# Performance work log

Hardware: AMD Instinct MI355X
Metric: run time of the kernel (lower is better)

The kernel has to match this reference:

```python
import jax, jax.numpy as jnp
import numpy as np

D = 256
H = 4
L = 6
N = 32768
VOCAB = 256
EPS = 1e-5  # torch LayerNorm default


def ln(x):
    # LayerNorm over last dim, no affine (elementwise_affine=False)
    m = x.mean(-1, keepdims=True)
    v = ((x - m) ** 2).mean(-1, keepdims=True)
    return (x - m) * jax.lax.rsqrt(v + EPS)


def rope(x):
    # standard rotary embedding over last dim (interleaved pairs), base 10000
    d = x.shape[-1]
    T = x.shape[-2]
    inv_freq = 1.0 / (10000.0 ** (jnp.arange(0, d, 2, dtype=jnp.float32) / d))
    ang = jnp.arange(T, dtype=jnp.float32)[:, None] * inv_freq[None, :]  # [T, d/2]
    cos, sin = jnp.cos(ang), jnp.sin(ang)
    x1, x2 = x[..., 0::2], x[..., 1::2]
    r1 = x1 * cos - x2 * sin
    r2 = x1 * sin + x2 * cos
    return jnp.stack([r1, r2], axis=-1).reshape(x.shape)


def setup_inputs() -> dict:
    key = jax.random.key(0)
    ks = jax.random.split(key, 6)
    B, T = 2, 1024
    idx = jax.random.randint(ks[0], (B, T), 0, VOCAB)
    std = 0.02
    wte = jax.random.normal(ks[1], (VOCAB, D), jnp.float32) * std
    encoder = jax.random.normal(ks[2], (N, D), jnp.float32) * std
    decoder_x = jax.random.normal(ks[3], (H, D, N // H), jnp.float32) * std
    decoder_y = jax.random.normal(ks[4], (H, D, N // H), jnp.float32) * std
    readout = jax.random.normal(ks[5], (D, VOCAB), jnp.float32) * std
    return {"idx": idx, "wte": wte, "encoder": encoder,
            "decoder_x": decoder_x, "decoder_y": decoder_y, "readout": readout}


def reference(idx, wte, encoder, decoder_x, decoder_y, readout):
    B, T = idx.shape
    v_ast = ln(wte[idx])[:, None]  # [B,1,T,D]
    # strictly-lower-triangular causal mask: tril(diagonal=-1)
    mask = jnp.tril(jnp.ones((T, T), dtype=bool), -1)
    for _ in range(L):
        # x: [B,H,T,N/H]
        x = jax.nn.relu(jnp.einsum('bltd,hdn->bhtn', v_ast, decoder_x))
        qr = rope(x)
        kr = rope(x)
        # raw dot-product scores, no softmax; strictly causal mask
        scores = jnp.einsum('bhtn,bhsn->bhts', qr, kr)  # [B,H,T,T]
        scores = jnp.where(mask, scores, 0.0)
        a_ast = jnp.einsum('bhts,blsd->bhtd', scores, v_ast)  # [B,H,T,D]
        y = jax.nn.relu(jnp.einsum('bhtd,hdn->bhtn', ln(a_ast), decoder_y)) * x
        y = jnp.transpose(y, (0, 2, 1, 3)).reshape(B, 1, T, N)  # [B,1,T,N]
        # dropout is identity in eval mode
        v_ast = ln(v_ast + ln(y @ encoder))
    return v_ast[:, 0] @ readout  # [B,T,VOCAB]
```

## Files before the change

### kernel.cpp

```cpp
#include <hip/hip_runtime.h>
#include <hip/hip_fp16.h>
#include <math.h>

#define D_     256
#define H_     4
#define NH     8192
#define NTOT   32768
#define T_     1024
#define B_     2
#define ROWS   2048
#define VOCAB_ 256
#define LAYERS 6
#define EPS_   1e-5f

typedef _Float16 f16;
typedef __attribute__((ext_vector_type(8))) _Float16 f16x8;
typedef __attribute__((ext_vector_type(4))) float f32x4;

#define BM 128
#define BN 128
#define BK 64
#define LDST (BK + 8)

#define EPI_F32       0
#define EPI_RELU      1
#define EPI_RELU_MUL  3
#define EPI_F32_ATOM  4
#define EPI_RELU_ROPE 5

__device__ __forceinline__ uint4 rope8(uint4 xin, uint4 csin) {
    union U { uint4 v; f16 h[8]; };
    U x, cs, o;
    x.v = xin; cs.v = csin;
#pragma unroll
    for (int j = 0; j < 4; j++) {
        float x1 = (float)x.h[2 * j], x2 = (float)x.h[2 * j + 1];
        float c  = (float)cs.h[2 * j], s = (float)cs.h[2 * j + 1];
        o.h[2 * j]     = (f16)(x1 * c - x2 * s);
        o.h[2 * j + 1] = (f16)(x1 * s + x2 * c);
    }
    return o.v;
}

template<int EPI, bool ROPE, bool ACVT>
__device__ __forceinline__ void gemm_core(
    const void* __restrict__ Av, int lda,
    const f16* __restrict__ Bt, int ldb,
    void* __restrict__ Cv, int ldc,
    int row0, int col0, int k0beg, int k_end,
    const f16* __restrict__ aux,
    const f16* __restrict__ cstab)
{
    __shared__ f16 As[BM * LDST];
    __shared__ f16 Bs[BN * LDST];

    const int tid  = threadIdx.x;
    const int lane = tid & 63;
    const int wid  = tid >> 6;
    const int wr   = (wid >> 1) * 64;
    const int wc   = (wid & 1) * 64;
    const int lr   = lane & 15;
    const int lk   = (lane >> 4) * 8;

    f32x4 acc[4][4];
#pragma unroll
    for (int m = 0; m < 4; m++)
#pragma unroll
        for (int n = 0; n < 4; n++) acc[m][n] = (f32x4){0.f, 0.f, 0.f, 0.f};

    for (int k0 = k0beg; k0 < k_end; k0 += BK) {
#pragma unroll
        for (int i = 0; i < 4; i++) {
            int v  = tid + i * 256;
            int r  = v >> 3;
            int c8 = (v & 7) << 3;
            uint4 av;
            if constexpr (ACVT) {
                const float* Af = (const float*)Av;
                size_t base = (size_t)(row0 + r) * lda + k0 + c8;
                float4 f0 = *(const float4*)(Af + base);
                float4 f1 = *(const float4*)(Af + base + 4);
                int colb = k0 + c8, row = row0 + r;
                float fv[8] = {f0.x, f0.y, f0.z, f0.w, f1.x, f1.y, f1.z, f1.w};
                union { uint4 v4; f16 h[8]; } u;
#pragma unroll
                for (int j = 0; j < 8; j++)
                    u.h[j] = (f16)((colb + j < row) ? fv[j] : 0.f);
                av = u.v4;
            } else {
                av = *(const uint4*)((const f16*)Av + (size_t)(row0 + r) * lda + k0 + c8);
                if constexpr (ROPE) {
                    int p = (k0 + c8) >> 1;
                    av = rope8(av, *(const uint4*)(cstab + ((size_t)(row0 + r) * 4096 + p) * 2));
                }
            }
            uint4 bv = *(const uint4*)(Bt + (size_t)(col0 + r) * ldb + k0 + c8);
            if constexpr (ROPE) {
                int p = (k0 + c8) >> 1;
                bv = rope8(bv, *(const uint4*)(cstab + ((size_t)(col0 + r) * 4096 + p) * 2));
            }
            *(uint4*)(&As[r * LDST + c8]) = av;
            *(uint4*)(&Bs[r * LDST + c8]) = bv;
        }
        __syncthreads();
#pragma unroll
        for (int kk = 0; kk < BK; kk += 32) {
            f16x8 af[4], bfr[4];
#pragma unroll
            for (int m = 0; m < 4; m++)
                af[m] = *(const f16x8*)(&As[(wr + m * 16 + lr) * LDST + kk + lk]);
#pragma unroll
            for (int n = 0; n < 4; n++)
                bfr[n] = *(const f16x8*)(&Bs[(wc + n * 16 + lr) * LDST + kk + lk]);
#pragma unroll
            for (int m = 0; m < 4; m++)
#pragma unroll
                for (int n = 0; n < 4; n++)
                    acc[m][n] = __builtin_amdgcn_mfma_f32_16x16x32_f16(
                        af[m], bfr[n], acc[m][n], 0, 0, 0);
        }
        __syncthreads();
    }

    const int rbase = (lane >> 4) * 4;
#pragma unroll
    for (int m = 0; m < 4; m++) {
#pragma unroll
        for (int n = 0; n < 4; n++) {
#pragma unroll
            for (int r = 0; r < 4; r++) {
                int row = row0 + wr + m * 16 + rbase + r;
                int col = col0 + wc + n * 16 + lr;
                float val = acc[m][n][r];
                size_t o = (size_t)row * ldc + col;
                if constexpr (EPI == EPI_F32) {
                    ((float*)Cv)[o] = val;
                } else if constexpr (EPI == EPI_RELU) {
                    ((f16*)Cv)[o] = (f16)(val > 0.f ? val : 0.f);
                } else if constexpr (EPI == EPI_RELU_MUL) {
                    float xv = (float)aux[o];
                    ((f16*)Cv)[o] = (f16)((val > 0.f ? val : 0.f) * xv);
                } else if constexpr (EPI == EPI_RELU_ROPE) {
                    float vr_ = val > 0.f ? val : 0.f;
                    float pr_ = __shfl_xor(vr_, 1);
                    int t = row & (T_ - 1);
                    int p = col >> 1;
                    union { unsigned u; f16 h[2]; } q;
                    q.u = *(const unsigned*)(cstab + ((size_t)t * 4096 + p) * 2);
                    float c = (float)q.h[0], s = (float)q.h[1];
                    float ro_ = (col & 1) ? (pr_ * s + vr_ * c) : (vr_ * c - pr_ * s);
                    ((f16*)Cv)[o] = (f16)vr_;
                    ((f16*)aux)[o] = (f16)ro_;
                } else {
                    atomicAdd(((float*)Cv) + o, val);
                }
            }
        }
    }
}

__global__ __launch_bounds__(256) void k_gemm_xr(const f16* __restrict__ vb,
                                                 const f16* __restrict__ dxTh,
                                                 f16* __restrict__ xh,
                                                 f16* __restrict__ qrh,
                                                 const f16* __restrict__ cstab)
{
    gemm_core<EPI_RELU_ROPE, false, false>(vb, D_, dxTh, D_, xh, NH,
                                           blockIdx.y * BM, blockIdx.x * BN,
                                           0, D_, qrh, cstab);
}

__global__ __launch_bounds__(256) void k_gemm_x(const f16* __restrict__ vb,
                                                const f16* __restrict__ dxTh,
                                                f16* __restrict__ xh)
{
    gemm_core<EPI_RELU, false, false>(vb, D_, dxTh, D_, xh, NH,
                                      blockIdx.y * BM, blockIdx.x * BN,
                                      0, D_, nullptr, nullptr);
}

#define KSPLIT_S 8
__global__ __launch_bounds__(256) void k_gemm_s2(const f16* __restrict__ qrh,
                                                 float* __restrict__ Sf)
{
    int tb = blockIdx.x;
    int b  = tb / 36, ti = tb % 36;
    int ty = 0;
    while ((ty + 1) * (ty + 2) / 2 <= ti) ty++;
    int tx = ti - ty * (ty + 1) / 2;
    int k0 = blockIdx.y * (NH / KSPLIT_S);
    const f16* Qb = qrh + (size_t)b * T_ * NH;
    gemm_core<EPI_F32_ATOM, false, false>(Qb, NH, Qb, NH,
                                          Sf + (size_t)b * T_ * T_, T_,
                                          ty * BM, tx * BN,
                                          k0, k0 + NH / KSPLIT_S, nullptr, nullptr);
}

__global__ __launch_bounds__(256) void k_gemm_s(const f16* __restrict__ xh,
                                                float* __restrict__ Sf,
                                                const f16* __restrict__ cstab)
{
    int tb = blockIdx.x;
    int b  = tb / 36, ti = tb % 36;
    int ty = 0;
    while ((ty + 1) * (ty + 2) / 2 <= ti) ty++;
    int tx = ti - ty * (ty + 1) / 2;
    int k0 = blockIdx.y * (NH / KSPLIT_S);
    const f16* Ab = xh + (size_t)b * T_ * NH;
    gemm_core<EPI_F32_ATOM, true, false>(Ab, NH, Ab, NH,
                                         Sf + (size_t)b * T_ * T_, T_,
                                         ty * BM, tx * BN,
                                         k0, k0 + NH / KSPLIT_S, nullptr, cstab);
}

#define CH_A 128
__global__ __launch_bounds__(256) void k_gemm_a(const float* __restrict__ Sf,
                                                const f16* __restrict__ vT,
                                                float* __restrict__ ah)
{
    int b = blockIdx.z >> 3, kc = blockIdx.z & 7;
    int kend = (blockIdx.y + 1) * BM;
    int k0 = kc * CH_A;
    if (k0 >= kend) return;
    gemm_core<EPI_F32_ATOM, false, true>(Sf + (size_t)b * T_ * T_, T_,
                                         vT + (size_t)b * D_ * T_, T_,
                                         ah + (size_t)b * T_ * D_, D_,
                                         blockIdx.y * BM, blockIdx.x * BN,
                                         k0, k0 + CH_A, nullptr, nullptr);
}

__global__ __launch_bounds__(256) void k_gemm_y(const f16* __restrict__ lnAh,
                                                const f16* __restrict__ dyTh,
                                                f16* __restrict__ xh)
{
    gemm_core<EPI_RELU_MUL, false, false>(lnAh, D_, dyTh, D_, xh, NH,
                                          blockIdx.y * BM, blockIdx.x * BN,
                                          0, D_, xh, nullptr);
}

#define KSPLIT_Z 16
__global__ __launch_bounds__(256) void k_gemm_z(const f16* __restrict__ yh,
                                                const f16* __restrict__ encTh,
                                                float* __restrict__ zb)
{
    int k0 = blockIdx.z * (NH / KSPLIT_Z);
    gemm_core<EPI_F32_ATOM, false, false>(yh, NH, encTh, NTOT, zb, D_,
                                          blockIdx.y * BM, blockIdx.x * BN,
                                          k0, k0 + NH / KSPLIT_Z, nullptr, nullptr);
}

__device__ __forceinline__ float wave_sum(float s) {
#pragma unroll
    for (int off = 32; off; off >>= 1) s += __shfl_xor(s, off);
    return s;
}

__device__ __forceinline__ float4 ln4(float4 x) {
    float m = wave_sum(x.x + x.y + x.z + x.w) * (1.f / 256.f);
    float d0 = x.x - m, d1 = x.y - m, d2 = x.z - m, d3 = x.w - m;
    float var = wave_sum(d0 * d0 + d1 * d1 + d2 * d2 + d3 * d3) * (1.f / 256.f);
    float rs = rsqrtf(var + EPS_);
    return make_float4(d0 * rs, d1 * rs, d2 * rs, d3 * rs);
}

__device__ __forceinline__ void store_v_row(float4 o, int row, int lane,
                                            float* v, f16* vb, f16* vT) {
    *(float4*)(v + (size_t)row * D_ + lane * 4) = o;
    union { unsigned long long u; f16 h[4]; } p;
    p.h[0] = (f16)o.x; p.h[1] = (f16)o.y; p.h[2] = (f16)o.z; p.h[3] = (f16)o.w;
    *(unsigned long long*)(vb + (size_t)row * D_ + lane * 4) = p.u;
    int b = row >> 10, t = row & (T_ - 1);
    f16* vtp = vT + ((size_t)b * D_ + lane * 4) * T_ + t;
    vtp[0] = p.h[0]; vtp[T_] = p.h[1]; vtp[2 * T_] = p.h[2]; vtp[3 * T_] = p.h[3];
}

__global__ __launch_bounds__(256) void k_embed_ln(const int* __restrict__ idx,
                                                  const float* __restrict__ wte,
                                                  float* __restrict__ v,
                                                  f16* __restrict__ vb,
                                                  f16* __restrict__ vT)
{
    int row = blockIdx.x * 4 + (threadIdx.x >> 6);
    int lane = threadIdx.x & 63;
    int tok = idx[row];
    float4 x = *(const float4*)(wte + (size_t)tok * D_ + lane * 4);
    store_v_row(ln4(x), row, lane, v, vb, vT);
}

__global__ __launch_bounds__(256) void k_ln_f16(const float* __restrict__ in,
                                                f16* __restrict__ out)
{
    int row = blockIdx.x * 4 + (threadIdx.x >> 6);
    int lane = threadIdx.x & 63;
    float4 x = *(const float4*)(in + (size_t)row * D_ + lane * 4);
    float4 o = ln4(x);
    union { unsigned long long u; f16 h[4]; } p;
    p.h[0] = (f16)o.x; p.h[1] = (f16)o.y; p.h[2] = (f16)o.z; p.h[3] = (f16)o.w;
    *(unsigned long long*)(out + (size_t)row * D_ + lane * 4) = p.u;
}

__global__ __launch_bounds__(256) void k_update(const float* __restrict__ z,
                                                float* __restrict__ v,
                                                f16* __restrict__ vb,
                                                f16* __restrict__ vT)
{
    int row = blockIdx.x * 4 + (threadIdx.x >> 6);
    int lane = threadIdx.x & 63;
    float4 zr = *(const float4*)(z + (size_t)row * D_ + lane * 4);
    float4 lz = ln4(zr);
    float4 vr = *(const float4*)(v + (size_t)row * D_ + lane * 4);
    float4 u = make_float4(vr.x + lz.x, vr.y + lz.y, vr.z + lz.z, vr.w + lz.w);
    store_v_row(ln4(u), row, lane, v, vb, vT);
}

__global__ __launch_bounds__(256) void k_tables(f16* __restrict__ cstab)
{
    int i = blockIdx.x * 256 + threadIdx.x;
    int t = i >> 12;
    int f = i & 4095;
    float invf = expf(-(float)f * (9.210340371976184f / 4096.f));
    float s, c;
    sincosf((float)t * invf, &s, &c);
    cstab[2 * i]     = (f16)c;
    cstab[2 * i + 1] = (f16)s;
}

__global__ void k_transpose(const float* __restrict__ in, f16* __restrict__ out,
                            int R, int C, size_t inBatch, size_t outBatch)
{
    const float* ip = in + (size_t)blockIdx.z * inBatch;
    f16* op = out + (size_t)blockIdx.z * outBatch;
    __shared__ float tile[32][33];
    int c0 = blockIdx.x * 32, r0 = blockIdx.y * 32;
    int tx = threadIdx.x, ty = threadIdx.y;
#pragma unroll
    for (int i = 0; i < 32; i += 8)
        tile[ty + i][tx] = ip[(size_t)(r0 + ty + i) * C + c0 + tx];
    __syncthreads();
#pragma unroll
    for (int i = 0; i < 32; i += 8)
        op[(size_t)(c0 + ty + i) * R + r0 + tx] = (f16)tile[tx][ty + i];
}

__global__ __launch_bounds__(256) void k_readout(const float* __restrict__ v,
                                                 const float* __restrict__ ro,
                                                 float* __restrict__ out)
{
    int row = blockIdx.x;
    int tid = threadIdx.x;
    __shared__ float vr[D_];
    vr[tid] = v[(size_t)row * D_ + tid];
    __syncthreads();
    float acc = 0.f;
#pragma unroll 8
    for (int d = 0; d < D_; d++) acc += vr[d] * ro[(size_t)d * VOCAB_ + tid];
    out[(size_t)row * VOCAB_ + tid] = acc;
}

__global__ void k_sentinel(float* out, float val) { out[0] = val; }

extern "C" void kernel_launch(void* const* d_in, const int* in_sizes, int n_in,
                              void* d_out, int out_size, void* d_ws, size_t ws_size,
                              hipStream_t stream)
{
    const int*   idx = (const int*)d_in[0];
    const float* wte = (const float*)d_in[1];
    const float* enc = (const float*)d_in[2];
    const float* dx  = (const float*)d_in[3];
    const float* dy  = (const float*)d_in[4];
    const float* ro  = (const float*)d_in[5];
    float* out = (float*)d_out;

    char* base = (char*)d_ws;
    size_t off = 0;
    auto alloc = [&](size_t bytes) -> void* {
        off = (off + 255) & ~(size_t)255;
        void* r = base + off;
        off += bytes;
        return r;
    };

    f16*   dxT   = (f16*)  alloc((size_t)H_ * NH * D_ * 2);
    f16*   dyT   = (f16*)  alloc((size_t)H_ * NH * D_ * 2);
    f16*   encT  = (f16*)  alloc((size_t)D_ * NTOT * 2);
    f16*   cstab = (f16*)  alloc((size_t)T_ * 4096 * 2 * 2);
    float* v     = (float*)alloc((size_t)ROWS * D_ * 4);
    f16*   vb    = (f16*)  alloc((size_t)ROWS * D_ * 2);
    f16*   vT    = (f16*)  alloc((size_t)B_ * D_ * T_ * 2);
    f16*   xh    = (f16*)  alloc((size_t)ROWS * NH * 2);
    float* Sf    = (float*)alloc((size_t)B_ * T_ * T_ * 4);
    float* ah    = (float*)alloc((size_t)ROWS * D_ * 4);
    f16*   lnAh  = (f16*)  alloc((size_t)ROWS * D_ * 2);
    float* zb    = (float*)alloc((size_t)ROWS * D_ * 4);
    size_t off_small = off;
    f16*   qrh   = (f16*)  alloc((size_t)ROWS * NH * 2);
    const bool bigws = (off <= ws_size);

    if (off_small > ws_size) {
        k_sentinel<<<1, 1, 0, stream>>>(out, 10000.f + (float)(ws_size >> 20));
        return;
    }

    dim3 blk(256), tb(32, 8);

    k_transpose<<<dim3(NH / 32, D_ / 32, H_), tb, 0, stream>>>(
        dx, dxT, D_, NH, (size_t)D_ * NH, (size_t)NH * D_);
    k_transpose<<<dim3(NH / 32, D_ / 32, H_), tb, 0, stream>>>(
        dy, dyT, D_, NH, (size_t)D_ * NH, (size_t)NH * D_);
    k_transpose<<<dim3(D_ / 32, NTOT / 32, 1), tb, 0, stream>>>(
        enc, encT, NTOT, D_, 0, 0);
    k_tables<<<T_ * 4096 / 256, blk, 0, stream>>>(cstab);
    k_embed_ln<<<ROWS / 4, blk, 0, stream>>>(idx, wte, v, vb, vT);

    for (int l = 0; l < LAYERS; l++) {
        hipMemsetAsync(zb, 0, (size_t)ROWS * D_ * 4, stream);
        for (int h = 0; h < H_; h++) {
            const f16* dxTh  = dxT + (size_t)h * NH * D_;
            const f16* dyTh  = dyT + (size_t)h * NH * D_;
            const f16* encTh = encT + (size_t)h * NH;
            if (bigws) {
                k_gemm_xr<<<dim3(NH / BN, ROWS / BM), blk, 0, stream>>>(
                    vb, dxTh, xh, qrh, cstab);
                hipMemsetAsync(Sf, 0, (size_t)B_ * T_ * T_ * 4, stream);
                k_gemm_s2<<<dim3(36 * B_, KSPLIT_S), blk, 0, stream>>>(qrh, Sf);
            } else {
                k_gemm_x<<<dim3(NH / BN, ROWS / BM), blk, 0, stream>>>(vb, dxTh, xh);
                hipMemsetAsync(Sf, 0, (size_t)B_ * T_ * T_ * 4, stream);
                k_gemm_s<<<dim3(36 * B_, KSPLIT_S), blk, 0, stream>>>(xh, Sf, cstab);
            }
            hipMemsetAsync(ah, 0, (size_t)ROWS * D_ * 4, stream);
            k_gemm_a<<<dim3(D_ / BN, T_ / BM, B_ * 8), blk, 0, stream>>>(Sf, vT, ah);
            k_ln_f16<<<ROWS / 4, blk, 0, stream>>>(ah, lnAh);
            k_gemm_y<<<dim3(NH / BN, ROWS / BM), blk, 0, stream>>>(lnAh, dyTh, xh);
            k_gemm_z<<<dim3(D_ / BN, ROWS / BM, KSPLIT_Z), blk, 0, stream>>>(xh, encTh, zb);
        }
        k_update<<<ROWS / 4, blk, 0, stream>>>(zb, v, vb, vT);
    }
    k_readout<<<ROWS, blk, 0, stream>>>(v, ro, out);
}
```

Before: 5.416 ms.

## Load GEMM tiles directly global-to-LDS with XOR-swizzled layout

Adds template flags so the plain f16 GEMM operand loads use the global_load_lds builtin, writing tiles straight into shared memory without passing through registers. The shared tile drops its padding and uses an XOR swizzle on 16-byte chunks to avoid bank conflicts, and the fragment reads apply the same swizzle. Operands that need conversion or RoPE keep the old register path. This aims to cut register pressure and load/store instruction overhead, at the cost of relying on the builtin's wave-contiguous destination semantics being correct.

```diff
diff --git a/kernel.cpp b/kernel.cpp
--- a/kernel.cpp
+++ b/kernel.cpp
@@ -42,7 +42,7 @@
     return o.v;
 }
 
-template<int EPI, bool ROPE, bool ACVT>
+template<int EPI, bool ROPE, bool ACVT, bool GA, bool GB>
 __device__ __forceinline__ void gemm_core(
     const void* __restrict__ Av, int lda,
     const f16* __restrict__ Bt, int ldb,
@@ -51,8 +51,10 @@
     const f16* __restrict__ aux,
     const f16* __restrict__ cstab)
 {
-    __shared__ f16 As[BM * LDST];
-    __shared__ f16 Bs[BN * LDST];
+    constexpr int SA = GA ? BK : LDST;
+    constexpr int SB = GB ? BK : LDST;
+    __shared__ f16 As[BM * SA];
+    __shared__ f16 Bs[BN * SB];
 
     const int tid  = threadIdx.x;
     const int lane = tid & 63;
@@ -73,45 +75,74 @@
         for (int i = 0; i < 4; i++) {
             int v  = tid + i * 256;
             int r  = v >> 3;
-            int c8 = (v & 7) << 3;
-            uint4 av;
-            if constexpr (ACVT) {
-                const float* Af = (const float*)Av;
-                size_t base = (size_t)(row0 + r) * lda + k0 + c8;
-                float4 f0 = *(const float4*)(Af + base);
-                float4 f1 = *(const float4*)(Af + base + 4);
-                int colb = k0 + c8, row = row0 + r;
-                float fv[8] = {f0.x, f0.y, f0.z, f0.w, f1.x, f1.y, f1.z, f1.w};
-                union { uint4 v4; f16 h[8]; } u;
-#pragma unroll
-                for (int j = 0; j < 8; j++)
-                    u.h[j] = (f16)((colb + j < row) ? fv[j] : 0.f);
-                av = u.v4;
+            if constexpr (GA) {
+                int cc = (((v & 7) ^ (r & 7)) << 3);
+                const f16* src = (const f16*)Av + (size_t)(row0 + r) * lda + k0 + cc;
+                __builtin_amdgcn_global_load_lds(
+                    (const __attribute__((address_space(1))) unsigned int*)src,
+                    (__attribute__((address_space(3))) unsigned int*)(As + (size_t)(v & ~63) * 8),
+                    16, 0, 0);
             } else {
-                av = *(const uint4*)((const f16*)Av + (size_t)(row0 + r) * lda + k0 + c8);
+                int c8 = (v & 7) << 3;
+                uint4 av;
+                if constexpr (ACVT) {
+                    const float* Af = (const float*)Av;
+                    size_t base = (size_t)(row0 + r) * lda + k0 + c8;
+                    float4 f0 = *(const float4*)(Af + base);
+                    float4 f1 = *(const float4*)(Af + base + 4);
+                    int colb = k0 + c8, row = row0 + r;
+                    float fv[8] = {f0.x, f0.y, f0.z, f0.w, f1.x, f1.y, f1.z, f1.w};
+                    union { uint4 v4; f16 h[8]; } u;
+#pragma unroll
+                    for (int j = 0; j < 8; j++)
+                        u.h[j] = (f16)((colb + j < row) ? fv[j] : 0.f);
+                    av = u.v4;
+                } else {
+                    av = *(const uint4*)((const f16*)Av + (size_t)(row0 + r) * lda + k0 + c8);
+                    if constexpr (ROPE) {
+                        int p = (k0 + c8) >> 1;
+                        av = rope8(av, *(const uint4*)(cstab + ((size_t)(row0 + r) * 4096 + p) * 2));
+                    }
+                }
+                *(uint4*)(&As[r * SA + c8]) = av;
+            }
+            if constexpr (GB) {
+                int cc = (((v & 7) ^ (r & 7)) << 3);
+                const f16* src = Bt + (size_t)(col0 + r) * ldb + k0 + cc;
+                __builtin_amdgcn_global_load_lds(
+                    (const __attribute__((address_space(1))) unsigned int*)src,
+                    (__attribute__((address_space(3))) unsigned int*)(Bs + (size_t)(v & ~63) * 8),
+                    16, 0, 0);
+            } else {
+                int c8 = (v & 7) << 3;
+                uint4 bv = *(const uint4*)(Bt + (size_t)(col0 + r) * ldb + k0 + c8);
                 if constexpr (ROPE) {
                     int p = (k0 + c8) >> 1;
-                    av = rope8(av, *(const uint4*)(cstab + ((size_t)(row0 + r) * 4096 + p) * 2));
+                    bv = rope8(bv, *(const uint4*)(cstab + ((size_t)(col0 + r) * 4096 + p) * 2));
                 }
-            }
-            uint4 bv = *(const uint4*)(Bt + (size_t)(col0 + r) * ldb + k0 + c8);
-            if constexpr (ROPE) {
-                int p = (k0 + c8) >> 1;
-                bv = rope8(bv, *(const uint4*)(cstab + ((size_t)(col0 + r) * 4096 + p) * 2));
-            }
-            *(uint4*)(&As[r * LDST + c8]) = av;
-            *(uint4*)(&Bs[r * LDST + c8]) = bv;
+                *(uint4*)(&Bs[r * SB + c8]) = bv;
+            }
         }
         __syncthreads();
 #pragma unroll
         for (int kk = 0; kk < BK; kk += 32) {
             f16x8 af[4], bfr[4];
 #pragma unroll
-            for (int m = 0; m < 4; m++)
-                af[m] = *(const f16x8*)(&As[(wr + m * 16 + lr) * LDST + kk + lk]);
-#pragma unroll
-            for (int n = 0; n < 4; n++)
-                bfr[n] = *(const f16x8*)(&Bs[(wc + n * 16 + lr) * LDST + kk + lk]);
+            for (int m = 0; m < 4; m++) {
+                int rr = wr + m * 16 + lr;
+                int off;
+                if constexpr (GA) off = ((((kk + lk) >> 3) ^ (rr & 7)) << 3);
+                else               off = kk + lk;
+                af[m] = *(const f16x8*)(&As[rr * SA + off]);
+            }
+#pragma unroll
+            for (int n = 0; n < 4; n++) {
+                int rr = wc + n * 16 + lr;
+                int off;
+                if constexpr (GB) off = ((((kk + lk) >> 3) ^ (rr & 7)) << 3);
+                else               off = kk + lk;
+                bfr[n] = *(const f16x8*)(&Bs[rr * SB + off]);
+            }
 #pragma unroll
             for (int m = 0; m < 4; m++)
 #pragma unroll
@@ -165,18 +196,18 @@
                                                  f16* __restrict__ qrh,
                                                  const f16* __restrict__ cstab)
 {
-    gemm_core<EPI_RELU_ROPE, false, false>(vb, D_, dxTh, D_, xh, NH,
-                                           blockIdx.y * BM, blockIdx.x * BN,
-                                           0, D_, qrh, cstab);
+    gemm_core<EPI_RELU_ROPE, false, false, true, true>(
+        vb, D_, dxTh, D_, xh, NH,
+        blockIdx.y * BM, blockIdx.x * BN, 0, D_, qrh, cstab);
 }
 
 __global__ __launch_bounds__(256) void k_gemm_x(const f16* __restrict__ vb,
                                                 const f16* __restrict__ dxTh,
                                                 f16* __restrict__ xh)
 {
-    gemm_core<EPI_RELU, false, false>(vb, D_, dxTh, D_, xh, NH,
-                                      blockIdx.y * BM, blockIdx.x * BN,
-                                      0, D_, nullptr, nullptr);
+    gemm_core<EPI_RELU, false, false, true, true>(
+        vb, D_, dxTh, D_, xh, NH,
+        blockIdx.y * BM, blockIdx.x * BN, 0, D_, nullptr, nullptr);
 }
 
 #define KSPLIT_S 8
@@ -190,10 +221,9 @@
     int tx = ti - ty * (ty + 1) / 2;
     int k0 = blockIdx.y * (NH / KSPLIT_S);
     const f16* Qb = qrh + (size_t)b * T_ * NH;
-    gemm_core<EPI_F32_ATOM, false, false>(Qb, NH, Qb, NH,
-                                          Sf + (size_t)b * T_ * T_, T_,
-                                          ty * BM, tx * BN,
-                                          k0, k0 + NH / KSPLIT_S, nullptr, nullptr);
+    gemm_core<EPI_F32_ATOM, false, false, true, true>(
+        Qb, NH, Qb, NH, Sf + (size_t)b * T_ * T_, T_,
+        ty * BM, tx * BN, k0, k0 + NH / KSPLIT_S, nullptr, nullptr);
 }
 
 __global__ __launch_bounds__(256) void k_gemm_s(const f16* __restrict__ xh,
@@ -207,10 +237,9 @@
     int tx = ti - ty * (ty + 1) / 2;
     int k0 = blockIdx.y * (NH / KSPLIT_S);
     const f16* Ab = xh + (size_t)b * T_ * NH;
-    gemm_core<EPI_F32_ATOM, true, false>(Ab, NH, Ab, NH,
-                                         Sf + (size_t)b * T_ * T_, T_,
-                                         ty * BM, tx * BN,
-                                         k0, k0 + NH / KSPLIT_S, nullptr, cstab);
+    gemm_core<EPI_F32_ATOM, true, false, false, false>(
+        Ab, NH, Ab, NH, Sf + (size_t)b * T_ * T_, T_,
+        ty * BM, tx * BN, k0, k0 + NH / KSPLIT_S, nullptr, cstab);
 }
 
 #define CH_A 128
@@ -222,20 +251,19 @@
     int kend = (blockIdx.y + 1) * BM;
     int k0 = kc * CH_A;
     if (k0 >= kend) return;
-    gemm_core<EPI_F32_ATOM, false, true>(Sf + (size_t)b * T_ * T_, T_,
-                                         vT + (size_t)b * D_ * T_, T_,
-                                         ah + (size_t)b * T_ * D_, D_,
-                                         blockIdx.y * BM, blockIdx.x * BN,
-                                         k0, k0 + CH_A, nullptr, nullptr);
+    gemm_core<EPI_F32_ATOM, false, true, false, true>(
+        Sf + (size_t)b * T_ * T_, T_, vT + (size_t)b * D_ * T_, T_,
+        ah + (size_t)b * T_ * D_, D_,
+        blockIdx.y * BM, blockIdx.x * BN, k0, k0 + CH_A, nullptr, nullptr);
 }
 
 __global__ __launch_bounds__(256) void k_gemm_y(const f16* __restrict__ lnAh,
                                                 const f16* __restrict__ dyTh,
                                                 f16* __restrict__ xh)
 {
-    gemm_core<EPI_RELU_MUL, false, false>(lnAh, D_, dyTh, D_, xh, NH,
-                                          blockIdx.y * BM, blockIdx.x * BN,
-                                          0, D_, xh, nullptr);
+    gemm_core<EPI_RELU_MUL, false, false, true, true>(
+        lnAh, D_, dyTh, D_, xh, NH,
+        blockIdx.y * BM, blockIdx.x * BN, 0, D_, xh, nullptr);
 }
 
 #define KSPLIT_Z 16
@@ -244,9 +272,9 @@
                                                 float* __restrict__ zb)
 {
     int k0 = blockIdx.z * (NH / KSPLIT_Z);
-    gemm_core<EPI_F32_ATOM, false, false>(yh, NH, encTh, NTOT, zb, D_,
-                                          blockIdx.y * BM, blockIdx.x * BN,
-                                          k0, k0 + NH / KSPLIT_Z, nullptr, nullptr);
+    gemm_core<EPI_F32_ATOM, false, false, true, true>(
+        yh, NH, encTh, NTOT, zb, D_,
+        blockIdx.y * BM, blockIdx.x * BN, k0, k0 + NH / KSPLIT_Z, nullptr, nullptr);
 }
 
 __device__ __forceinline__ float wave_sum(float s) {
```

Result: faster. 4.439 ms (-18.1%).
